# Optimization experiments

Measured on AMD Instinct MI355X. Metric: run time of the kernel, lower is better.

The kernel has to match this reference:

```python
import jax, jax.numpy as jnp
import numpy as np

B, S_X, S_Y = 2, 2048, 2048
C1, C2, H, D, W_EXP = 1024, 1024, 16, 64, 4
EPS = 1e-5


def _layernorm(x, w, b):
    mu = jnp.mean(x, axis=-1, keepdims=True)
    var = jnp.mean(jnp.square(x - mu), axis=-1, keepdims=True)
    return (x - mu) * jax.lax.rsqrt(var + EPS) * w + b


def setup_inputs() -> dict:
    key = jax.random.key(0)
    ks = jax.random.split(key, 12)
    s = lambda fan_in: 1.0 / np.sqrt(fan_in)
    inp = {
        "x": jax.random.normal(ks[0], (B, S_X, C1), jnp.float32),
        "y": jax.random.normal(ks[1], (B, S_Y, C2), jnp.float32),
        # per-head projections, batched over heads: [H, in, d]
        "Wq": jax.random.uniform(ks[2], (H, C1, D), jnp.float32, -s(C1), s(C1)),
        "Wk": jax.random.uniform(ks[3], (H, C2, D), jnp.float32, -s(C2), s(C2)),
        "Wv": jax.random.uniform(ks[4], (H, C2, D), jnp.float32, -s(C2), s(C2)),
        "li1_w": jax.random.uniform(ks[5], (H * D, C1), jnp.float32, -s(H * D), s(H * D)),
        "li1_b": jax.random.uniform(ks[6], (C1,), jnp.float32, -s(H * D), s(H * D)),
        "ln1_w": jnp.ones((C1,), jnp.float32),
        "ln1_b": jnp.zeros((C1,), jnp.float32),
        "ln2_w": jnp.ones((C2,), jnp.float32),
        "ln2_b": jnp.zeros((C2,), jnp.float32),
        "ln3_w": jnp.ones((C1,), jnp.float32),
        "ln3_b": jnp.zeros((C1,), jnp.float32),
        "li2_w": jax.random.uniform(ks[7], (C1, C1 * W_EXP), jnp.float32, -s(C1), s(C1)),
        "li2_b": jax.random.uniform(ks[8], (C1 * W_EXP,), jnp.float32, -s(C1), s(C1)),
        "li3_w": jax.random.uniform(ks[9], (C1 * W_EXP, C1), jnp.float32, -s(C1 * W_EXP), s(C1 * W_EXP)),
        "li3_b": jax.random.uniform(ks[10], (C1,), jnp.float32, -s(C1 * W_EXP), s(C1 * W_EXP)),
    }
    return inp


def reference(x, y, Wq, Wk, Wv, li1_w, li1_b, ln1_w, ln1_b, ln2_w, ln2_b,
              ln3_w, ln3_b, li2_w, li2_b, li3_w, li3_b):
    xn = _layernorm(x, ln1_w, ln1_b)            # [B, Sx, C1]
    yn = _layernorm(y, ln2_w, ln2_b)            # [B, Sy, C2]
    # batched per-head projections (original loops over 16 Head modules)
    q = jnp.einsum("bsc,hcd->bhsd", xn, Wq)
    k = jnp.einsum("btc,hcd->bhtd", yn, Wk)
    v = jnp.einsum("btc,hcd->bhtd", yn, Wv)
    a = jnp.einsum("bhsd,bhtd->bhst", q, k) * (D ** -0.5)
    a = jax.nn.softmax(a, axis=-1)
    # faithful to original: triu(diagonal=1) applied AFTER softmax (zeros diag too)
    mask = jnp.triu(jnp.ones((S_X, S_Y), bool), k=1)
    a = jnp.where(mask, a, 0.0)
    o = jnp.einsum("bhst,bhtd->bhsd", a, v)     # [B, H, Sx, D]
    o = o.transpose(0, 2, 1, 3).reshape(B, S_X, H * D)  # concat heads
    x_out = x + o @ li1_w + li1_b
    h = _layernorm(x_out, ln3_w, ln3_b)
    h = jax.nn.gelu(h @ li2_w + li2_b, approximate=False)
    h = h @ li3_w + li3_b
    return x_out + h
```

## Files before the change

kernel.cpp:

```cpp
#include <hip/hip_runtime.h>
#include <hip/hip_bf16.h>


typedef __hip_bfloat16 bf16;
typedef __attribute__((ext_vector_type(8))) short  s16x8;
typedef __attribute__((ext_vector_type(4))) short  s16x4;
typedef __attribute__((ext_vector_type(4))) float  f32x4;
typedef __attribute__((ext_vector_type(4))) _Float16 h16x4;

__device__ __forceinline__ float bfbits2f(short s) {
    return __uint_as_float(((unsigned)(unsigned short)s) << 16);
}
__device__ __forceinline__ float load_in(const void* p, size_t i, int f32) {
    return f32 ? ((const float*)p)[i] : bfbits2f(((const short*)p)[i]);
}
__device__ __forceinline__ void async16(const short* g, short* l) {
    __builtin_amdgcn_global_load_lds(
        (const __attribute__((address_space(1))) void*)g,
        (__attribute__((address_space(3))) void*)l, 16, 0, 0);
}

__global__ __launch_bounds__(256)
void detect_dtype(const short* __restrict__ x, int* __restrict__ flag)
{
    const int tid = threadIdx.x;
    int cnt = 0;
#pragma unroll
    for (int e = 0; e < 16; e++) {
        int idx = (tid * 16 + e) * 2;
        int ex  = (x[idx] >> 7) & 0xFF;
        if (ex >= 113 && ex <= 142) cnt++;
    }
#pragma unroll
    for (int off = 1; off < 64; off <<= 1) cnt += __shfl_xor(cnt, off, 64);
    __shared__ int sh[4];
    if ((tid & 63) == 0) sh[tid >> 6] = cnt;
    __syncthreads();
    if (tid == 0) {
        int tot = sh[0] + sh[1] + sh[2] + sh[3];
        flag[0] = (tot < 2458) ? 1 : 0;
    }
}

__global__ __launch_bounds__(256)
void conv_bias3(const void* b1, const void* b2, const void* b3,
                bf16* o1, bf16* o2, bf16* o3, const int* __restrict__ flag)
{
    const int f32 = flag[0];
    int i = blockIdx.x * 256 + threadIdx.x;
    if (i < 1024)      o1[i]        = __float2bfloat16(load_in(b1, i, f32));
    else if (i < 5120) o2[i - 1024] = __float2bfloat16(load_in(b2, i - 1024, f32));
    else               o3[i - 5120] = __float2bfloat16(load_in(b3, i - 5120, f32));
}

__global__ __launch_bounds__(256)
void transpose_tiled(const void* __restrict__ in, bf16* __restrict__ out,
                     int R, int Cc, const int* __restrict__ flag)
{
    __shared__ float tile[32][33];
    const int f32 = flag[0];
    const int tx = threadIdx.x & 31, ty = threadIdx.x >> 5;
    const int c0 = blockIdx.x * 32, r0 = blockIdx.y * 32;
#pragma unroll
    for (int i = 0; i < 4; i++)
        tile[ty + i * 8][tx] = load_in(in, (size_t)(r0 + ty + i * 8) * Cc + c0 + tx, f32);
    __syncthreads();
#pragma unroll
    for (int i = 0; i < 4; i++)
        out[(size_t)(c0 + ty + i * 8) * R + r0 + tx] = __float2bfloat16(tile[tx][ty + i * 8]);
}

__global__ __launch_bounds__(256)
void pack_qkv_tiled(const void* __restrict__ in, bf16* __restrict__ out,
                    const int* __restrict__ flag)
{
    __shared__ float tile[32][33];
    const int f32 = flag[0];
    const int tx = threadIdx.x & 31, ty = threadIdx.x >> 5;
    const int c0 = blockIdx.x * 32, r0 = blockIdx.y * 32;
    const size_t base = (size_t)blockIdx.z * 1024 * 64;
#pragma unroll
    for (int i = 0; i < 4; i++)
        tile[ty + i * 8][tx] = load_in(in, base + (size_t)(r0 + ty + i * 8) * 64 + c0 + tx, f32);
    __syncthreads();
#pragma unroll
    for (int i = 0; i < 4; i++)
        out[base + (size_t)(c0 + ty + i * 8) * 1024 + r0 + tx] =
            __float2bfloat16(tile[tx][ty + i * 8]);
}

__global__ __launch_bounds__(256)
void ln_kernel(const void* __restrict__ x, const void* __restrict__ w,
               const void* __restrict__ bv, bf16* __restrict__ out,
               const int* __restrict__ flag, int x_is_bf16,
               bf16* __restrict__ copy_out)
{
    const int f32  = flag[0];
    const int xf32 = x_is_bf16 ? 0 : f32;
    const int row  = blockIdx.x;
    const int tid  = threadIdx.x;
    const int lane = tid & 63;
    const int wave = tid >> 6;
    const size_t base = (size_t)row * 1024 + tid * 4;

    float v[4];
    float sum = 0.f, ss = 0.f;
#pragma unroll
    for (int e = 0; e < 4; e++) {
        v[e] = load_in(x, base + e, xf32);
        sum += v[e]; ss += v[e] * v[e];
    }
    if (copy_out) {
        s16x4 c;
#pragma unroll
        for (int e = 0; e < 4; e++) {
            __hip_bfloat16 hb = __float2bfloat16(v[e]);
            c[e] = *(short*)&hb;
        }
        *(s16x4*)((short*)copy_out + base) = c;
    }
#pragma unroll
    for (int off = 1; off < 64; off <<= 1) {
        sum += __shfl_xor(sum, off, 64);
        ss  += __shfl_xor(ss,  off, 64);
    }
    __shared__ float sh1[4], sh2[4];
    if (lane == 0) { sh1[wave] = sum; sh2[wave] = ss; }
    __syncthreads();
    float t1 = sh1[0] + sh1[1] + sh1[2] + sh1[3];
    float t2 = sh2[0] + sh2[1] + sh2[2] + sh2[3];
    float mu   = t1 * (1.f / 1024.f);
    float var  = t2 * (1.f / 1024.f) - mu * mu;
    float rstd = rsqrtf(var + 1e-5f);

#pragma unroll
    for (int e = 0; e < 4; e++) {
        float ov = (v[e] - mu) * rstd * load_in(w, tid * 4 + e, f32)
                 + load_in(bv, tid * 4 + e, f32);
        out[base + e] = __float2bfloat16(ov);
    }
}

template<int BN>
__global__ __launch_bounds__(256)
void gemm_bt(const bf16* __restrict__ A, const bf16* __restrict__ Bt,
             const bf16* __restrict__ bias, const bf16* __restrict__ res,
             void* __restrict__ C, int M, int N, int K, int act,
             const int* __restrict__ dflag, int final_out)
{
    constexpr int JN = BN / 32;
    __shared__ alignas(16) short As[128][32];
    __shared__ alignas(16) short Bs[BN][32];

    const int f32out = final_out ? dflag[0] : 0;
    const int tid  = threadIdx.x;
    const int lane = tid & 63;
    const int wave = tid >> 6;
    const int q    = lane >> 4;
    const int l15  = lane & 15;
    const int wm   = (wave >> 1) * 64;
    const int wn   = (wave & 1) * (BN / 2);
    const int bm   = blockIdx.x * 128;
    const int bn   = blockIdx.y * BN;

    const int lr = lane >> 2;
    const int lc = (lane & 3) * 8;

    f32x4 acc[4][JN] = {};

    const short* Abase = (const short*)A  + (size_t)(bm + wave * 32 + lr) * K + lc;
    const short* Bbase;
    if (BN == 128) Bbase = (const short*)Bt + (size_t)(bn + wave * 32 + lr) * K + lc;
    else           Bbase = (const short*)Bt + (size_t)(bn + wave * 16 + lr) * K + lc;

    for (int k0 = 0; k0 < K; k0 += 32) {
        __syncthreads();
        async16(Abase + k0,                  &As[wave * 32][0]);
        async16(Abase + k0 + (size_t)16 * K, &As[wave * 32 + 16][0]);
        if (BN == 128) {
            async16(Bbase + k0,                  &Bs[wave * 32][0]);
            async16(Bbase + k0 + (size_t)16 * K, &Bs[wave * 32 + 16][0]);
        } else {
            async16(Bbase + k0, &Bs[wave * 16][0]);
        }
        __syncthreads();

        s16x8 af[4], bfrag[JN];
#pragma unroll
        for (int i = 0; i < 4; i++)  af[i]    = *(const s16x8*)&As[wm + i * 16 + l15][q * 8];
#pragma unroll
        for (int j = 0; j < JN; j++) bfrag[j] = *(const s16x8*)&Bs[wn + j * 16 + l15][q * 8];
#pragma unroll
        for (int i = 0; i < 4; i++)
#pragma unroll
            for (int j = 0; j < JN; j++)
                acc[i][j] = __builtin_amdgcn_mfma_f32_16x16x32_bf16(af[i], bfrag[j], acc[i][j], 0, 0, 0);
    }

#pragma unroll
    for (int i = 0; i < 4; i++) {
#pragma unroll
        for (int j = 0; j < JN; j++) {
            int n = bn + wn + j * 16 + l15;
            float bvv = bias ? __bfloat162float(bias[n]) : 0.f;
#pragma unroll
            for (int r = 0; r < 4; r++) {
                int m = bm + wm + i * 16 + q * 4 + r;
                float v = acc[i][j][r] + bvv;
                if (act) v = 0.5f * v * (1.f + erff(v * 0.70710678118f));
                if (res) v += __bfloat162float(res[(size_t)m * N + n]);
                size_t idx = (size_t)m * N + n;
                if (f32out) ((float*)C)[idx] = v;
                else        ((bf16*)C)[idx]  = __float2bfloat16(v);
            }
        }
    }
}

__global__ __launch_bounds__(256)
void gemm_bt64(const bf16* __restrict__ A, const bf16* __restrict__ Bt,
               const bf16* __restrict__ bias, const bf16* __restrict__ res,
               void* __restrict__ C, int M, int N, int K, int act,
               const int* __restrict__ dflag, int final_out)
{
    __shared__ alignas(16) short As[128][64];
    __shared__ alignas(16) short Bs[64][64];

    const int f32out = final_out ? dflag[0] : 0;
    const int tid  = threadIdx.x;
    const int lane = tid & 63;
    const int wave = tid >> 6;
    const int q    = lane >> 4;
    const int l15  = lane & 15;
    const int wm   = (wave >> 1) * 64;
    const int wn   = (wave & 1) * 32;
    const int bm   = blockIdx.x * 128;
    const int bn   = blockIdx.y * 64;

    const int srow   = lane >> 3;
    const int gchunk = (lane & 7) ^ srow;
    const short* Ab = (const short*)A  + (size_t)(bm + wave * 32 + srow) * K + gchunk * 8;
    const short* Bb = (const short*)Bt + (size_t)(bn + wave * 16 + srow) * K + gchunk * 8;
    const int csw = l15 & 7;

    f32x4 acc[4][2] = {};

    for (int k0 = 0; k0 < K; k0 += 64) {
        __syncthreads();
        async16(Ab + k0,                  &As[wave * 32][0]);
        async16(Ab + k0 + (size_t)8  * K, &As[wave * 32 + 8][0]);
        async16(Ab + k0 + (size_t)16 * K, &As[wave * 32 + 16][0]);
        async16(Ab + k0 + (size_t)24 * K, &As[wave * 32 + 24][0]);
        async16(Bb + k0,                  &Bs[wave * 16][0]);
        async16(Bb + k0 + (size_t)8  * K, &Bs[wave * 16 + 8][0]);
        __syncthreads();

        s16x8 af[4][2], bfr[2][2];
#pragma unroll
        for (int i = 0; i < 4; i++)
#pragma unroll
            for (int kk = 0; kk < 2; kk++)
                af[i][kk] = *(const s16x8*)&As[wm + i * 16 + l15][((kk * 4 + q) ^ csw) * 8];
#pragma unroll
        for (int j = 0; j < 2; j++)
#pragma unroll
            for (int kk = 0; kk < 2; kk++)
                bfr[j][kk] = *(const s16x8*)&Bs[wn + j * 16 + l15][((kk * 4 + q) ^ csw) * 8];
#pragma unroll
        for (int i = 0; i < 4; i++)
#pragma unroll
            for (int j = 0; j < 2; j++) {
                acc[i][j] = __builtin_amdgcn_mfma_f32_16x16x32_bf16(af[i][0], bfr[j][0], acc[i][j], 0, 0, 0);
                acc[i][j] = __builtin_amdgcn_mfma_f32_16x16x32_bf16(af[i][1], bfr[j][1], acc[i][j], 0, 0, 0);
            }
    }

#pragma unroll
    for (int i = 0; i < 4; i++) {
#pragma unroll
        for (int j = 0; j < 2; j++) {
            int n = bn + wn + j * 16 + l15;
            float bvv = bias ? __bfloat162float(bias[n]) : 0.f;
#pragma unroll
            for (int r = 0; r < 4; r++) {
                int m = bm + wm + i * 16 + q * 4 + r;
                float v = acc[i][j][r] + bvv;
                if (act) v = 0.5f * v * (1.f + erff(v * 0.70710678118f));
                if (res) v += __bfloat162float(res[(size_t)m * N + n]);
                size_t idx = (size_t)m * N + n;
                if (f32out) ((float*)C)[idx] = v;
                else        ((bf16*)C)[idx]  = __float2bfloat16(v);
            }
        }
    }
}

__global__ __launch_bounds__(256)
void attn_kernel(const bf16* __restrict__ Q, const bf16* __restrict__ KV,
                 bf16* __restrict__ O)
{
    __shared__ alignas(16) short    Ks[64][72];
    __shared__ alignas(16) _Float16 Vs[64][72];

    const int tid  = threadIdx.x;
    const int lane = tid & 63;
    const int wave = tid >> 6;
    const int q    = lane >> 4;
    const int l15  = lane & 15;
    const int bh   = blockIdx.y;
    const int b    = bh >> 4, h = bh & 15;
    const int sblk   = blockIdx.x * 64;
    const int s_base = sblk + wave * 16;
    const int s_glob = s_base + l15;

    const short* qrow = (const short*)Q + (size_t)(b * 2048 + s_glob) * 1024 + h * 64;
    s16x8 qf0 = *(const s16x8*)(qrow + q * 8);
    s16x8 qf1 = *(const s16x8*)(qrow + 32 + q * 8);

    float l_lane = 0.f;
    f32x4 o_acc[4] = {};

    const int trow   = tid >> 2;
    const int tchunk = tid & 3;
    const int kswz   = (tchunk ^ (trow >> 2)) & 3;
    const int vcol   = (((trow >> 4) ^ tchunk) & 3) * 16 + (trow & 15);
    const int ksw    = l15 >> 2;

    for (int t0 = 0; t0 < 2048; t0 += 64) {
        const bool needV = (t0 >= sblk);
        const short* krow = (const short*)KV + (size_t)(b * 2048 + t0 + trow) * 2048 + h * 64;
        s16x8 k0 = *(const s16x8*)(krow + tchunk * 16);
        s16x8 k1 = *(const s16x8*)(krow + tchunk * 16 + 8);
        s16x8 v0, v1;
        if (needV) {
            const short* vrow = krow + 1024;
            v0 = *(const s16x8*)(vrow + tchunk * 16);
            v1 = *(const s16x8*)(vrow + tchunk * 16 + 8);
        }
        __syncthreads();
        *(s16x8*)&Ks[trow][kswz * 16]     = k0;
        *(s16x8*)&Ks[trow][kswz * 16 + 8] = k1;
        if (needV) {
#pragma unroll
            for (int e = 0; e < 8; e++) {
                Vs[tchunk * 16 + e][vcol]     = (_Float16)bfbits2f(v0[e]);
                Vs[tchunk * 16 + 8 + e][vcol] = (_Float16)bfbits2f(v1[e]);
            }
        }
        __syncthreads();

#pragma unroll
        for (int sub = 0; sub < 4; sub++) {
            const int tb  = sub * 16;
            const int rel = t0 + tb - s_base;
            s16x8 kf0 = *(const s16x8*)&Ks[tb + l15][(((q >> 1) ^ ksw) & 3) * 16 + (q & 1) * 8];
            s16x8 kf1 = *(const s16x8*)&Ks[tb + l15][((((q >> 1) + 2) ^ ksw) & 3) * 16 + (q & 1) * 8];
            f32x4 st = {};
            st = __builtin_amdgcn_mfma_f32_16x16x32_bf16(kf0, qf0, st, 0, 0, 0);
            st = __builtin_amdgcn_mfma_f32_16x16x32_bf16(kf1, qf1, st, 0, 0, 0);
            float p[4];
#pragma unroll
            for (int r = 0; r < 4; r++) {
                float sc = st[r] * 0.125f;
                p[r] = __expf(fminf(sc, 60.f));
                l_lane += p[r];
            }
            if (rel >= 0) {
                h16x4 pf;
                if (rel == 0) {
#pragma unroll
                    for (int r = 0; r < 4; r++)
                        pf[r] = (q * 4 + r > l15) ? (_Float16)p[r] : (_Float16)0.f;
                } else {
#pragma unroll
                    for (int r = 0; r < 4; r++) pf[r] = (_Float16)p[r];
                }
#pragma unroll
                for (int dt = 0; dt < 4; dt++) {
                    h16x4 vf = *(const h16x4*)&Vs[dt * 16 + l15]
                                                 [(((tb >> 4) ^ dt) & 3) * 16 + q * 4];
                    o_acc[dt] = __builtin_amdgcn_mfma_f32_16x16x16f16(pf, vf, o_acc[dt], 0, 0, 0);
                }
            }
        }
    }

    float l = l_lane;
    l += __shfl_xor(l, 16, 64);
    l += __shfl_xor(l, 32, 64);
    float linv[4];
#pragma unroll
    for (int r = 0; r < 4; r++) linv[r] = 1.f / __shfl(l, q * 4 + r, 64);
#pragma unroll
    for (int dt = 0; dt < 4; dt++)
#pragma unroll
        for (int r = 0; r < 4; r++) {
            int s = s_base + q * 4 + r;
            int d = dt * 16 + l15;
            O[(size_t)(b * 2048 + s) * 1024 + h * 64 + d] =
                __float2bfloat16(o_acc[dt][r] * linv[r]);
        }
}

extern "C" void kernel_launch(void* const* d_in, const int* in_sizes, int n_in,
                              void* d_out, int out_size, void* d_ws, size_t ws_size,
                              hipStream_t stream)
{
    const void* x     = d_in[0];
    const void* y     = d_in[1];
    const void* Wq    = d_in[2];
    const void* Wk    = d_in[3];
    const void* Wv    = d_in[4];
    const void* li1_w = d_in[5];
    const void* li1_b = d_in[6];
    const void* ln1_w = d_in[7];
    const void* ln1_b = d_in[8];
    const void* ln2_w = d_in[9];
    const void* ln2_b = d_in[10];
    const void* ln3_w = d_in[11];
    const void* ln3_b = d_in[12];
    const void* li2_w = d_in[13];
    const void* li2_b = d_in[14];
    const void* li3_w = d_in[15];
    const void* li3_b = d_in[16];

    char* w = (char*)d_ws;
    const size_t MB = 1u << 20;
    bf16* xn    = (bf16*)(w + 0 * MB);
    bf16* yn    = (bf16*)(w + 8 * MB);
    bf16* WqT   = (bf16*)(w + 16 * MB);
    bf16* WkT   = (bf16*)(w + 18 * MB);
    bf16* WvT   = (bf16*)(w + 20 * MB);
    bf16* li1T  = (bf16*)(w + 22 * MB);
    bf16* li2T  = (bf16*)(w + 24 * MB);
    bf16* li3T  = (bf16*)(w + 32 * MB);
    bf16* xout  = (bf16*)(w + 40 * MB);
    bf16* Qb    = (bf16*)(w + 48 * MB);
    bf16* KVb   = (bf16*)(w + 56 * MB);
    bf16* h2    = (bf16*)(w + 48 * MB);
    bf16* xc    = (bf16*)(w + 80 * MB);
    int*  flag  = (int*) (w + 88 * MB);
    bf16* li1bc = (bf16*)(w + 88 * MB + 4096);
    bf16* li2bc = (bf16*)(w + 88 * MB + 8192);
    bf16* li3bc = (bf16*)(w + 88 * MB + 24576);
    bf16* Ob    = yn;
    bf16* hn    = xn;

    detect_dtype<<<1, 256, 0, stream>>>((const short*)x, flag);

    conv_bias3<<<24, 256, 0, stream>>>(li1_b, li2_b, li3_b, li1bc, li2bc, li3bc, flag);

    ln_kernel<<<4096, 256, 0, stream>>>(x, ln1_w, ln1_b, xn, flag, 0, xc);
    ln_kernel<<<4096, 256, 0, stream>>>(y, ln2_w, ln2_b, yn, flag, 0, nullptr);

    pack_qkv_tiled<<<dim3(2, 32, 16), 256, 0, stream>>>(Wq, WqT, flag);
    pack_qkv_tiled<<<dim3(2, 32, 16), 256, 0, stream>>>(Wk, WkT, flag);
    pack_qkv_tiled<<<dim3(2, 32, 16), 256, 0, stream>>>(Wv, WvT, flag);
    transpose_tiled<<<dim3(32, 32),  256, 0, stream>>>(li1_w, li1T, 1024, 1024, flag);
    transpose_tiled<<<dim3(128, 32), 256, 0, stream>>>(li2_w, li2T, 1024, 4096, flag);
    transpose_tiled<<<dim3(32, 128), 256, 0, stream>>>(li3_w, li3T, 4096, 1024, flag);

    gemm_bt64<<<dim3(32, 16), 256, 0, stream>>>(xn, WqT, nullptr, nullptr, Qb, 4096, 1024, 1024, 0, flag, 0);
    gemm_bt64<<<dim3(32, 32), 256, 0, stream>>>(yn, WkT, nullptr, nullptr, KVb, 4096, 2048, 1024, 0, flag, 0);

    attn_kernel<<<dim3(32, 32), 256, 0, stream>>>(Qb, KVb, Ob);

    gemm_bt64<<<dim3(32, 16), 256, 0, stream>>>(Ob, li1T, li1bc, xc, xout, 4096, 1024, 1024, 0, flag, 0);

    ln_kernel<<<4096, 256, 0, stream>>>(xout, ln3_w, ln3_b, hn, flag, 1, nullptr);

    gemm_bt<128><<<dim3(32, 32), 256, 0, stream>>>(hn, li2T, li2bc, nullptr, h2, 4096, 4096, 1024, 1, flag, 0);

    gemm_bt64<<<dim3(32, 16), 256, 0, stream>>>(h2, li3T, li3bc, xout, d_out, 4096, 1024, 4096, 0, flag, 1);
}
```

Before: 524.6 us.

## Pre-transpose V to fp16 and use async swizzled LDS loads in attention and MLP GEMM

Adds a kernel that transposes V once into an fp16 [d, t] buffer. The attention kernel can then stage K and V tiles with direct global-to-LDS async loads under an XOR swizzle, replacing register loads and scattered per-element LDS writes. Separately, the 128x128 GEMM for the MLP up-projection now uses a K-step of 64 with XOR-swizzled LDS, which halves the number of barrier pairs. The cost is an extra kernel launch plus the extra global traffic to write and read the Vt buffer.

```diff
diff --git a/kernel.cpp b/kernel.cpp
--- a/kernel.cpp
+++ b/kernel.cpp
@@ -87,6 +87,23 @@
     for (int i = 0; i < 4; i++)
         out[base + (size_t)(c0 + ty + i * 8) * 1024 + r0 + tx] =
             __float2bfloat16(tile[tx][ty + i * 8]);
+}
+
+__global__ __launch_bounds__(256)
+void v_transpose(const bf16* __restrict__ KV, _Float16* __restrict__ Vt)
+{
+    __shared__ short tile[32][33];
+    const int tx = threadIdx.x & 31, ty = threadIdx.x >> 5;
+    const int t0 = blockIdx.x * 32, hd0 = blockIdx.y * 32, b = blockIdx.z;
+#pragma unroll
+    for (int i = 0; i < 4; i++)
+        tile[ty + i * 8][tx] =
+            ((const short*)KV)[(size_t)(b * 2048 + t0 + ty + i * 8) * 2048 + 1024 + hd0 + tx];
+    __syncthreads();
+#pragma unroll
+    for (int i = 0; i < 4; i++)
+        Vt[(size_t)(b * 1024 + hd0 + ty + i * 8) * 2048 + t0 + tx] =
+            (_Float16)bfbits2f(tile[tx][ty + i * 8]);
 }
 
 __global__ __launch_bounds__(256)
@@ -138,82 +155,6 @@
         float ov = (v[e] - mu) * rstd * load_in(w, tid * 4 + e, f32)
                  + load_in(bv, tid * 4 + e, f32);
         out[base + e] = __float2bfloat16(ov);
-    }
-}
-
-template<int BN>
-__global__ __launch_bounds__(256)
-void gemm_bt(const bf16* __restrict__ A, const bf16* __restrict__ Bt,
-             const bf16* __restrict__ bias, const bf16* __restrict__ res,
-             void* __restrict__ C, int M, int N, int K, int act,
-             const int* __restrict__ dflag, int final_out)
-{
-    constexpr int JN = BN / 32;
-    __shared__ alignas(16) short As[128][32];
-    __shared__ alignas(16) short Bs[BN][32];
-
-    const int f32out = final_out ? dflag[0] : 0;
-    const int tid  = threadIdx.x;
-    const int lane = tid & 63;
-    const int wave = tid >> 6;
-    const int q    = lane >> 4;
-    const int l15  = lane & 15;
-    const int wm   = (wave >> 1) * 64;
-    const int wn   = (wave & 1) * (BN / 2);
-    const int bm   = blockIdx.x * 128;
-    const int bn   = blockIdx.y * BN;
-
-    const int lr = lane >> 2;
-    const int lc = (lane & 3) * 8;
-
-    f32x4 acc[4][JN] = {};
-
-    const short* Abase = (const short*)A  + (size_t)(bm + wave * 32 + lr) * K + lc;
-    const short* Bbase;
-    if (BN == 128) Bbase = (const short*)Bt + (size_t)(bn + wave * 32 + lr) * K + lc;
-    else           Bbase = (const short*)Bt + (size_t)(bn + wave * 16 + lr) * K + lc;
-
-    for (int k0 = 0; k0 < K; k0 += 32) {
-        __syncthreads();
-        async16(Abase + k0,                  &As[wave * 32][0]);
-        async16(Abase + k0 + (size_t)16 * K, &As[wave * 32 + 16][0]);
-        if (BN == 128) {
-            async16(Bbase + k0,                  &Bs[wave * 32][0]);
-            async16(Bbase + k0 + (size_t)16 * K, &Bs[wave * 32 + 16][0]);
-        } else {
-            async16(Bbase + k0, &Bs[wave * 16][0]);
-        }
-        __syncthreads();
-
-        s16x8 af[4], bfrag[JN];
-#pragma unroll
-        for (int i = 0; i < 4; i++)  af[i]    = *(const s16x8*)&As[wm + i * 16 + l15][q * 8];
-#pragma unroll
-        for (int j = 0; j < JN; j++) bfrag[j] = *(const s16x8*)&Bs[wn + j * 16 + l15][q * 8];
-#pragma unroll
-        for (int i = 0; i < 4; i++)
-#pragma unroll
-            for (int j = 0; j < JN; j++)
-                acc[i][j] = __builtin_amdgcn_mfma_f32_16x16x32_bf16(af[i], bfrag[j], acc[i][j], 0, 0, 0);
-    }
-
-#pragma unroll
-    for (int i = 0; i < 4; i++) {
-#pragma unroll
-        for (int j = 0; j < JN; j++) {
-            int n = bn + wn + j * 16 + l15;
-            float bvv = bias ? __bfloat162float(bias[n]) : 0.f;
-#pragma unroll
-            for (int r = 0; r < 4; r++) {
-                int m = bm + wm + i * 16 + q * 4 + r;
-                float v = acc[i][j][r] + bvv;
-                if (act) v = 0.5f * v * (1.f + erff(v * 0.70710678118f));
-                if (res) v += __bfloat162float(res[(size_t)m * N + n]);
-                size_t idx = (size_t)m * N + n;
-                if (f32out) ((float*)C)[idx] = v;
-                else        ((bf16*)C)[idx]  = __float2bfloat16(v);
-            }
-        }
     }
 }
 
@@ -296,11 +237,83 @@
 }
 
 __global__ __launch_bounds__(256)
+void gemm_bt128(const bf16* __restrict__ A, const bf16* __restrict__ Bt,
+                const bf16* __restrict__ bias, const bf16* __restrict__ res,
+                void* __restrict__ C, int M, int N, int K, int act,
+                const int* __restrict__ dflag, int final_out)
+{
+    __shared__ alignas(16) short As[128][64];
+    __shared__ alignas(16) short Bs[128][64];
+
+    const int f32out = final_out ? dflag[0] : 0;
+    const int tid  = threadIdx.x;
+    const int lane = tid & 63;
+    const int wave = tid >> 6;
+    const int q    = lane >> 4;
+    const int l15  = lane & 15;
+    const int wm   = (wave >> 1) * 64;
+    const int wn   = (wave & 1) * 64;
+    const int bm   = blockIdx.x * 128;
+    const int bn   = blockIdx.y * 128;
+
+    const int srow   = lane >> 3;
+    const int gchunk = (lane & 7) ^ srow;
+    const short* Ab = (const short*)A  + (size_t)(bm + wave * 32 + srow) * K + gchunk * 8;
+    const short* Bb = (const short*)Bt + (size_t)(bn + wave * 32 + srow) * K + gchunk * 8;
+    const int csw = l15 & 7;
+
+    f32x4 acc[4][4] = {};
+
+    for (int k0 = 0; k0 < K; k0 += 64) {
+        __syncthreads();
+#pragma unroll
+        for (int r8 = 0; r8 < 4; r8++) {
+            async16(Ab + k0 + (size_t)(r8 * 8) * K, &As[wave * 32 + r8 * 8][0]);
+            async16(Bb + k0 + (size_t)(r8 * 8) * K, &Bs[wave * 32 + r8 * 8][0]);
+        }
+        __syncthreads();
+
+#pragma unroll
+        for (int kk = 0; kk < 2; kk++) {
+            s16x8 af[4], bfr[4];
+#pragma unroll
+            for (int i = 0; i < 4; i++) af[i]  = *(const s16x8*)&As[wm + i * 16 + l15][((kk * 4 + q) ^ csw) * 8];
+#pragma unroll
+            for (int j = 0; j < 4; j++) bfr[j] = *(const s16x8*)&Bs[wn + j * 16 + l15][((kk * 4 + q) ^ csw) * 8];
+#pragma unroll
+            for (int i = 0; i < 4; i++)
+#pragma unroll
+                for (int j = 0; j < 4; j++)
+                    acc[i][j] = __builtin_amdgcn_mfma_f32_16x16x32_bf16(af[i], bfr[j], acc[i][j], 0, 0, 0);
+        }
+    }
+
+#pragma unroll
+    for (int i = 0; i < 4; i++) {
+#pragma unroll
+        for (int j = 0; j < 4; j++) {
+            int n = bn + wn + j * 16 + l15;
+            float bvv = bias ? __bfloat162float(bias[n]) : 0.f;
+#pragma unroll
+            for (int r = 0; r < 4; r++) {
+                int m = bm + wm + i * 16 + q * 4 + r;
+                float v = acc[i][j][r] + bvv;
+                if (act) v = 0.5f * v * (1.f + erff(v * 0.70710678118f));
+                if (res) v += __bfloat162float(res[(size_t)m * N + n]);
+                size_t idx = (size_t)m * N + n;
+                if (f32out) ((float*)C)[idx] = v;
+                else        ((bf16*)C)[idx]  = __float2bfloat16(v);
+            }
+        }
+    }
+}
+
+__global__ __launch_bounds__(256)
 void attn_kernel(const bf16* __restrict__ Q, const bf16* __restrict__ KV,
-                 bf16* __restrict__ O)
-{
-    __shared__ alignas(16) short    Ks[64][72];
-    __shared__ alignas(16) _Float16 Vs[64][72];
+                 const _Float16* __restrict__ Vt, bf16* __restrict__ O)
+{
+    __shared__ alignas(16) short    Ks[64][64];
+    __shared__ alignas(16) _Float16 Vs[64][64];
 
     const int tid  = threadIdx.x;
     const int lane = tid & 63;
@@ -320,32 +333,24 @@
     float l_lane = 0.f;
     f32x4 o_acc[4] = {};
 
-    const int trow   = tid >> 2;
-    const int tchunk = tid & 3;
-    const int kswz   = (tchunk ^ (trow >> 2)) & 3;
-    const int vcol   = (((trow >> 4) ^ tchunk) & 3) * 16 + (trow & 15);
-    const int ksw    = l15 >> 2;
+    const int srow = lane >> 3;
+    const int gch  = (lane & 7) ^ srow;
+    const short*    kbase = (const short*)KV +
+        (size_t)(b * 2048 + wave * 16 + srow) * 2048 + h * 64 + gch * 8;
+    const _Float16* vbase = Vt +
+        (size_t)(b * 1024 + h * 64 + wave * 16 + srow) * 2048 + gch * 8;
+    const int key = l15 & 7;
 
     for (int t0 = 0; t0 < 2048; t0 += 64) {
         const bool needV = (t0 >= sblk);
-        const short* krow = (const short*)KV + (size_t)(b * 2048 + t0 + trow) * 2048 + h * 64;
-        s16x8 k0 = *(const s16x8*)(krow + tchunk * 16);
-        s16x8 k1 = *(const s16x8*)(krow + tchunk * 16 + 8);
-        s16x8 v0, v1;
+        const short*    kg = kbase + (size_t)t0 * 2048;
+        const _Float16* vg = vbase + t0;
+        __syncthreads();
+        async16(kg,                    &Ks[wave * 16][0]);
+        async16(kg + (size_t)8 * 2048, &Ks[wave * 16 + 8][0]);
         if (needV) {
-            const short* vrow = krow + 1024;
-            v0 = *(const s16x8*)(vrow + tchunk * 16);
-            v1 = *(const s16x8*)(vrow + tchunk * 16 + 8);
-        }
-        __syncthreads();
-        *(s16x8*)&Ks[trow][kswz * 16]     = k0;
-        *(s16x8*)&Ks[trow][kswz * 16 + 8] = k1;
-        if (needV) {
-#pragma unroll
-            for (int e = 0; e < 8; e++) {
-                Vs[tchunk * 16 + e][vcol]     = (_Float16)bfbits2f(v0[e]);
-                Vs[tchunk * 16 + 8 + e][vcol] = (_Float16)bfbits2f(v1[e]);
-            }
+            async16((const short*)vg,                    (short*)&Vs[wave * 16][0]);
+            async16((const short*)(vg + (size_t)8 * 2048), (short*)&Vs[wave * 16 + 8][0]);
         }
         __syncthreads();
 
@@ -353,8 +358,8 @@
         for (int sub = 0; sub < 4; sub++) {
             const int tb  = sub * 16;
             const int rel = t0 + tb - s_base;
-            s16x8 kf0 = *(const s16x8*)&Ks[tb + l15][(((q >> 1) ^ ksw) & 3) * 16 + (q & 1) * 8];
-            s16x8 kf1 = *(const s16x8*)&Ks[tb + l15][((((q >> 1) + 2) ^ ksw) & 3) * 16 + (q & 1) * 8];
+            s16x8 kf0 = *(const s16x8*)&Ks[tb + l15][(q ^ key) * 8];
+            s16x8 kf1 = *(const s16x8*)&Ks[tb + l15][((q + 4) ^ key) * 8];
             f32x4 st = {};
             st = __builtin_amdgcn_mfma_f32_16x16x32_bf16(kf0, qf0, st, 0, 0, 0);
             st = __builtin_amdgcn_mfma_f32_16x16x32_bf16(kf1, qf1, st, 0, 0, 0);
@@ -378,7 +383,7 @@
 #pragma unroll
                 for (int dt = 0; dt < 4; dt++) {
                     h16x4 vf = *(const h16x4*)&Vs[dt * 16 + l15]
-                                                 [(((tb >> 4) ^ dt) & 3) * 16 + q * 4];
+                        [(((2 * sub + (q >> 1)) ^ key) * 8) + (q & 1) * 4];
                     o_acc[dt] = __builtin_amdgcn_mfma_f32_16x16x16f16(pf, vf, o_acc[dt], 0, 0, 0);
                 }
             }
@@ -437,6 +442,7 @@
     bf16* xout  = (bf16*)(w + 40 * MB);
     bf16* Qb    = (bf16*)(w + 48 * MB);
     bf16* KVb   = (bf16*)(w + 56 * MB);
+    _Float16* Vt = (_Float16*)(w + 72 * MB);
     bf16* h2    = (bf16*)(w + 48 * MB);
     bf16* xc    = (bf16*)(w + 80 * MB);
     int*  flag  = (int*) (w + 88 * MB);
@@ -462,14 +468,15 @@
 
     gemm_bt64<<<dim3(32, 16), 256, 0, stream>>>(xn, WqT, nullptr, nullptr, Qb, 4096, 1024, 1024, 0, flag, 0);
     gemm_bt64<<<dim3(32, 32), 256, 0, stream>>>(yn, WkT, nullptr, nullptr, KVb, 4096, 2048, 1024, 0, flag, 0);
-
-    attn_kernel<<<dim3(32, 32), 256, 0, stream>>>(Qb, KVb, Ob);
+    v_transpose<<<dim3(64, 32, 2), 256, 0, stream>>>(KVb, Vt);
+
+    attn_kernel<<<dim3(32, 32), 256, 0, stream>>>(Qb, KVb, Vt, Ob);
 
     gemm_bt64<<<dim3(32, 16), 256, 0, stream>>>(Ob, li1T, li1bc, xc, xout, 4096, 1024, 1024, 0, flag, 0);
 
     ln_kernel<<<4096, 256, 0, stream>>>(xout, ln3_w, ln3_b, hn, flag, 1, nullptr);
 
-    gemm_bt<128><<<dim3(32, 32), 256, 0, stream>>>(hn, li2T, li2bc, nullptr, h2, 4096, 4096, 1024, 1, flag, 0);
+    gemm_bt128<<<dim3(32, 32), 256, 0, stream>>>(hn, li2T, li2bc, nullptr, h2, 4096, 4096, 1024, 1, flag, 0);
 
     gemm_bt64<<<dim3(32, 16), 256, 0, stream>>>(h2, li3T, li3bc, xout, d_out, 4096, 1024, 4096, 0, flag, 1);
 }
```

Measured after the change: 502.6 us. 4.2% less time.
